# Kernel optimization log

Hardware: AMD Instinct MI355X
Metric: run time of the kernel (lower is better)

## Reference

```python
import jax, jax.numpy as jnp
import numpy as np

B, L, E, H = 1, 2048, 512, 8
D = E // H


def setup_inputs() -> dict:
    key = jax.random.key(0)
    k0, k1, k2 = jax.random.split(key, 3)
    x = jax.random.normal(k0, (B, L, E), jnp.float32)
    W_qkv = jax.random.normal(k1, (E, 3 * E), jnp.float32) / np.sqrt(E).astype(np.float32)
    b_qkv = jnp.zeros((3 * E,), jnp.float32)
    W_out = jax.random.normal(k2, (E, E), jnp.float32) / np.sqrt(E).astype(np.float32)
    b_out = jnp.zeros((E,), jnp.float32)
    return {"x": x, "W_qkv": W_qkv, "b_qkv": b_qkv, "W_out": W_out, "b_out": b_out}


def reference(x, W_qkv, b_qkv, W_out, b_out):
    num_heads = H
    eps = 1e-6
    b, l, e = x.shape
    d = e // num_heads
    qkv = x @ W_qkv + b_qkv                      # [B, L, 3E]
    q, k, v = jnp.split(qkv, 3, axis=-1)
    q = q.reshape(b, l, num_heads, d).transpose(0, 2, 1, 3)  # [B,H,L,D]
    k = k.reshape(b, l, num_heads, d).transpose(0, 2, 1, 3)
    v = v.reshape(b, l, num_heads, d).transpose(0, 2, 1, 3)
    pos = jnp.arange(l, dtype=jnp.float32).reshape(1, 1, l, 1)
    cos_w = jnp.cos(jnp.pi / 2 * pos / l)
    sin_w = jnp.sin(jnp.pi / 2 * pos / l)
    q_prime = jax.nn.relu(q)
    k_prime = jax.nn.relu(k)

    def branch(w):
        qw = q_prime * w                          # [B,H,L,D]
        kw = k_prime * w
        kv = jnp.einsum('bhld,bhle->bhlde', kw, v)  # causal running KV state
        kv_cum = jnp.cumsum(kv, axis=2)
        ctx = jnp.einsum('bhld,bhlde->bhle', qw, kv_cum)
        nrm = jnp.einsum('bhld,bhld->bhl', qw, jnp.cumsum(kw, axis=2))
        return ctx, nrm

    ctx_cos, nrm_cos = branch(cos_w)
    ctx_sin, nrm_sin = branch(sin_w)
    out = (ctx_cos + ctx_sin) / ((nrm_cos + nrm_sin)[..., None] + eps)
    out = out.transpose(0, 2, 1, 3).reshape(b, l, e)
    return out @ W_out + b_out
```

## Files before the change

kernel.cpp:

```cpp
#include <hip/hip_runtime.h>

constexpr int L_SEQ = 2048;
constexpr int E_DIM = 512;
constexpr int H_NUM = 8;
constexpr int QKV_W = 3 * E_DIM;
constexpr int CHK = 64;
constexpr int NC = L_SEQ / CHK;
constexpr float PI_HALF = 1.5707963267948966f;

typedef __attribute__((ext_vector_type(8))) short bf16x8;
typedef __attribute__((ext_vector_type(4))) float f32x4;
typedef __attribute__((ext_vector_type(4))) short short4v;

__device__ __forceinline__ short f2bf(float f) {
  union { float f; unsigned int u; } v; v.f = f;
  unsigned int r = v.u + 0x7fffu + ((v.u >> 16) & 1u);
  return (short)(r >> 16);
}
__device__ __forceinline__ float bf2f(short s) {
  union { unsigned int u; float f; } v;
  v.u = ((unsigned int)(unsigned short)s) << 16;
  return v.f;
}

__device__ __forceinline__ void glds16(const void* g, void* l) {
  __builtin_amdgcn_global_load_lds(
      (const __attribute__((address_space(1))) unsigned int*)g,
      (__attribute__((address_space(3))) unsigned int*)l, 16, 0, 0);
}

template <int WTM, int WTN>
__global__ __launch_bounds__(256) void gemm_mfma_bf16(
    const short* __restrict__ A, const short* __restrict__ Bt,
    const float* __restrict__ bias, float* __restrict__ C,
    int M, int N, int K) {
  constexpr int BM = WTM * 32;
  constexpr int BN = WTN * 32;
  __shared__ short As[BM * 32];
  __shared__ short Bs[BN * 32];

  const int t = threadIdx.x;
  const int wave = t >> 6;
  const int lane = t & 63;
  const int quad = lane >> 4;
  const int lr = lane & 15;

  const int row0 = blockIdx.y * BM;
  const int col0 = blockIdx.x * BN;
  const int wrow = (wave >> 1) * (BM / 2);
  const int wcol = (wave & 1) * (BN / 2);

  f32x4 acc[WTM][WTN];
#pragma unroll
  for (int m = 0; m < WTM; ++m)
#pragma unroll
    for (int n = 0; n < WTN; ++n) acc[m][n] = (f32x4){0.f, 0.f, 0.f, 0.f};

  for (int k0 = 0; k0 < K; k0 += 32) {
#pragma unroll
    for (int p = wave; p < BM / 16; p += 4) {
      const int idx = p * 64 + lane;
      const int r = idx >> 2;
      const int kq = (idx & 3) * 8;
      glds16(A + (size_t)(row0 + r) * K + k0 + kq, As + p * 512);
    }
#pragma unroll
    for (int p = wave; p < BN / 16; p += 4) {
      const int idx = p * 64 + lane;
      const int r = idx >> 2;
      const int kq = (idx & 3) * 8;
      glds16(Bt + (size_t)(col0 + r) * K + k0 + kq, Bs + p * 512);
    }
    __syncthreads();

    bf16x8 af[WTM], bf_[WTN];
#pragma unroll
    for (int m = 0; m < WTM; ++m)
      af[m] = *(const bf16x8*)(As + (wrow + m * 16 + lr) * 32 + quad * 8);
#pragma unroll
    for (int n = 0; n < WTN; ++n)
      bf_[n] = *(const bf16x8*)(Bs + (wcol + n * 16 + lr) * 32 + quad * 8);
#pragma unroll
    for (int m = 0; m < WTM; ++m)
#pragma unroll
      for (int n = 0; n < WTN; ++n)
        acc[m][n] = __builtin_amdgcn_mfma_f32_16x16x32_bf16(af[m], bf_[n], acc[m][n], 0, 0, 0);
    __syncthreads();
  }

#pragma unroll
  for (int m = 0; m < WTM; ++m) {
#pragma unroll
    for (int n = 0; n < WTN; ++n) {
      const int col = col0 + wcol + n * 16 + lr;
      const int rowb = row0 + wrow + m * 16 + quad * 4;
      const float bb = bias[col];
#pragma unroll
      for (int r = 0; r < 4; ++r)
        C[(size_t)(rowb + r) * N + col] = acc[m][n][r] + bb;
    }
  }
}

__global__ __launch_bounds__(256) void cast_x_kernel(
    const float* __restrict__ x, short* __restrict__ xb) {
  const int i = blockIdx.x * 256 + threadIdx.x;
  const float4 v = ((const float4*)x)[i];
  short4v o;
  o.x = f2bf(v.x); o.y = f2bf(v.y); o.z = f2bf(v.z); o.w = f2bf(v.w);
  ((short4v*)xb)[i] = o;
}

__global__ __launch_bounds__(256) void transpose_cast_kernel(
    const float* __restrict__ W, short* __restrict__ Wt, int R, int Cc) {
  __shared__ float tile[32][33];
  const int c0 = blockIdx.x * 32, r0 = blockIdx.y * 32;
  const int tx = threadIdx.x & 31, ty = threadIdx.x >> 5;
  for (int i = ty; i < 32; i += 8) tile[i][tx] = W[(size_t)(r0 + i) * Cc + c0 + tx];
  __syncthreads();
  for (int i = ty; i < 32; i += 8)
    Wt[(size_t)(c0 + i) * R + r0 + tx] = f2bf(tile[tx][i]);
}

__global__ __launch_bounds__(256) void chunk_kv_mfma(
    const float* __restrict__ qkv, float* __restrict__ S, float* __restrict__ ksum) {
  const int c = blockIdx.x, h = blockIdx.y;
  __shared__ short kT[128][72];
  __shared__ short vT[64][72];
  const int t = threadIdx.x;
  const int w = t >> 6, lane = t & 63, lr = lane & 15, quad = lane >> 4;

#pragma unroll
  for (int r = 0; r < 16; ++r) {
    const int i = w + 4 * r, d = lane;
    const float* row = qkv + (size_t)(c * 64 + i) * QKV_W;
    const float kv_ = fmaxf(row[E_DIM + h * 64 + d], 0.f);
    const float v_ = row[2 * E_DIM + h * 64 + d];
    const float th = PI_HALF * (float)(c * 64 + i) / (float)L_SEQ;
    kT[d][i] = f2bf(kv_ * __cosf(th));
    kT[64 + d][i] = f2bf(kv_ * __sinf(th));
    vT[d][i] = f2bf(v_);
  }
  __syncthreads();

  f32x4 acc[8];
#pragma unroll
  for (int n = 0; n < 8; ++n) acc[n] = (f32x4){0.f, 0.f, 0.f, 0.f};
#pragma unroll
  for (int kk = 0; kk < 2; ++kk) {
    const bf16x8 av = *(const bf16x8*)&vT[16 * w + lr][kk * 32 + quad * 8];
#pragma unroll
    for (int n = 0; n < 8; ++n) {
      const bf16x8 bv = *(const bf16x8*)&kT[16 * n + lr][kk * 32 + quad * 8];
      acc[n] = __builtin_amdgcn_mfma_f32_16x16x32_bf16(av, bv, acc[n], 0, 0, 0);
    }
  }

  float* Sc = S + ((size_t)(h * NC + c)) * 8192;
#pragma unroll
  for (int n = 0; n < 8; ++n) {
    const int dd = 16 * n + lr;
#pragma unroll
    for (int r = 0; r < 4; ++r) {
      const int e = 16 * w + quad * 4 + r;
      Sc[(size_t)e * 128 + dd] = acc[n][r];
    }
  }

  if (t < 128) {
    float s = 0.f;
#pragma unroll
    for (int j = 0; j < 8; ++j) {
      const bf16x8 kv8 = *(const bf16x8*)&kT[t][j * 8];
#pragma unroll
      for (int q = 0; q < 8; ++q) s += bf2f(kv8[q]);
    }
    ksum[(size_t)(h * NC + c) * 128 + t] = s;
  }
}

__global__ __launch_bounds__(256) void scan_kernel(
    const float* __restrict__ S, short* __restrict__ Spb,
    const float* __restrict__ ksum, float* __restrict__ ksumP) {
  const int h = blockIdx.y;
  const int e = blockIdx.x * 256 + threadIdx.x;
  float run = 0.f;
#pragma unroll
  for (int c = 0; c < NC; ++c) {
    const size_t off = ((size_t)(h * NC + c)) * 8192 + e;
    Spb[off] = f2bf(run);
    run += S[off];
  }
  if (blockIdx.x == 0 && threadIdx.x < 128) {
    const int d = threadIdx.x;
    float r2 = 0.f;
#pragma unroll
    for (int c = 0; c < NC; ++c) {
      const size_t off = (size_t)(h * NC + c) * 128 + d;
      ksumP[off] = r2;
      r2 += ksum[off];
    }
  }
}

__global__ __launch_bounds__(256) void chunk_out_mfma(
    const float* __restrict__ qkv, const short* __restrict__ Spb,
    const float* __restrict__ ksumP, short* __restrict__ attn) {
  const int c = blockIdx.x, h = blockIdx.y;
  __shared__ short Qc[64][136];
  __shared__ short Kc[64][136];
  __shared__ short Am[64][72];
  __shared__ short vT[64][72];
  __shared__ float nrmP[64][4];
  __shared__ float nrmA[64];
  const int t = threadIdx.x;
  const int w = t >> 6, lane = t & 63, lr = lane & 15, quad = lane >> 4;

#pragma unroll
  for (int r = 0; r < 16; ++r) {
    const int i = w + 4 * r, d = lane;
    const float* row = qkv + (size_t)(c * 64 + i) * QKV_W;
    const float q_ = fmaxf(row[h * 64 + d], 0.f);
    const float k_ = fmaxf(row[E_DIM + h * 64 + d], 0.f);
    const float v_ = row[2 * E_DIM + h * 64 + d];
    const float th = PI_HALF * (float)(c * 64 + i) / (float)L_SEQ;
    const float cw = __cosf(th), sw = __sinf(th);
    Qc[i][d] = f2bf(q_ * cw);
    Qc[i][64 + d] = f2bf(q_ * sw);
    Kc[i][d] = f2bf(k_ * cw);
    Kc[i][64 + d] = f2bf(k_ * sw);
    vT[d][i] = f2bf(v_);
  }
  __syncthreads();

  f32x4 acc_a[4];
#pragma unroll
  for (int n = 0; n < 4; ++n) acc_a[n] = (f32x4){0.f, 0.f, 0.f, 0.f};
#pragma unroll
  for (int kk = 0; kk < 4; ++kk) {
    const bf16x8 av = *(const bf16x8*)&Qc[16 * w + lr][kk * 32 + quad * 8];
#pragma unroll
    for (int n = 0; n < 4; ++n) {
      const bf16x8 bv = *(const bf16x8*)&Kc[16 * n + lr][kk * 32 + quad * 8];
      acc_a[n] = __builtin_amdgcn_mfma_f32_16x16x32_bf16(av, bv, acc_a[n], 0, 0, 0);
    }
  }
#pragma unroll
  for (int n = 0; n < 4; ++n) {
#pragma unroll
    for (int r = 0; r < 4; ++r) {
      const int gi = 16 * w + quad * 4 + r;
      const int gj = 16 * n + lr;
      float val = (gj <= gi) ? acc_a[n][r] : 0.f;
      Am[gi][gj] = f2bf(val);
      float s = val;
      s += __shfl_xor(s, 1, 64);
      s += __shfl_xor(s, 2, 64);
      s += __shfl_xor(s, 4, 64);
      s += __shfl_xor(s, 8, 64);
      if (lr == 0) nrmP[gi][n] = s;
    }
  }

  const short* Spc = Spb + ((size_t)(h * NC + c)) * 8192;
  f32x4 acc_c[4];
#pragma unroll
  for (int n = 0; n < 4; ++n) acc_c[n] = (f32x4){0.f, 0.f, 0.f, 0.f};
#pragma unroll
  for (int kk = 0; kk < 4; ++kk) {
    const bf16x8 av = *(const bf16x8*)&Qc[16 * w + lr][kk * 32 + quad * 8];
#pragma unroll
    for (int n = 0; n < 4; ++n) {
      const bf16x8 bv = *(const bf16x8*)(Spc + (size_t)(16 * n + lr) * 128 + kk * 32 + quad * 8);
      acc_c[n] = __builtin_amdgcn_mfma_f32_16x16x32_bf16(av, bv, acc_c[n], 0, 0, 0);
    }
  }
  __syncthreads();

#pragma unroll
  for (int kk = 0; kk < 2; ++kk) {
    const bf16x8 av = *(const bf16x8*)&Am[16 * w + lr][kk * 32 + quad * 8];
#pragma unroll
    for (int n = 0; n < 4; ++n) {
      const bf16x8 bv = *(const bf16x8*)&vT[16 * n + lr][kk * 32 + quad * 8];
      acc_c[n] = __builtin_amdgcn_mfma_f32_16x16x32_bf16(av, bv, acc_c[n], 0, 0, 0);
    }
  }

  {
    const int i = t >> 2, p = t & 3;
    const float* Kp = ksumP + (size_t)(h * NC + c) * 128;
    float dot = 0.f;
#pragma unroll
    for (int jj = 0; jj < 32; ++jj) {
      const int dd = p * 32 + jj;
      dot += bf2f(Qc[i][dd]) * Kp[dd];
    }
    nrmP[i][p] += dot;
  }
  __syncthreads();
  if (t < 64) nrmA[t] = nrmP[t][0] + nrmP[t][1] + nrmP[t][2] + nrmP[t][3];
  __syncthreads();

#pragma unroll
  for (int n = 0; n < 4; ++n) {
#pragma unroll
    for (int r = 0; r < 4; ++r) {
      const int gi = 16 * w + quad * 4 + r;
      const int e = 16 * n + lr;
      const float val = acc_c[n][r] / (nrmA[gi] + 1e-6f);
      attn[(size_t)(c * 64 + gi) * E_DIM + h * 64 + e] = f2bf(val);
    }
  }
}

extern "C" void kernel_launch(void* const* d_in, const int* in_sizes, int n_in,
                              void* d_out, int out_size, void* d_ws, size_t ws_size,
                              hipStream_t stream) {
  (void)in_sizes; (void)n_in; (void)out_size; (void)ws_size;
  const float* x     = (const float*)d_in[0];
  const float* W_qkv = (const float*)d_in[1];
  const float* b_qkv = (const float*)d_in[2];
  const float* W_out = (const float*)d_in[3];
  const float* b_out = (const float*)d_in[4];
  float* out = (float*)d_out;

  float* ws = (float*)d_ws;
  float* qkv    = ws;
  float* S      = qkv + 3145728;
  float* ksum   = S + 2097152;
  float* ksumP  = ksum + 32768;
  short* Spb    = (short*)(ksumP + 32768);
  short* attn_b = Spb + 2097152;
  short* xb     = attn_b + 1048576;
  short* Wqkv_t = xb + 1048576;
  short* Wout_t = Wqkv_t + 786432;

  cast_x_kernel<<<1024, 256, 0, stream>>>(x, xb);
  transpose_cast_kernel<<<dim3(48, 16), 256, 0, stream>>>(W_qkv, Wqkv_t, E_DIM, QKV_W);
  transpose_cast_kernel<<<dim3(16, 16), 256, 0, stream>>>(W_out, Wout_t, E_DIM, E_DIM);

  gemm_mfma_bf16<4, 4><<<dim3(QKV_W / 128, L_SEQ / 128), 256, 0, stream>>>(
      xb, Wqkv_t, b_qkv, qkv, L_SEQ, QKV_W, E_DIM);

  chunk_kv_mfma<<<dim3(NC, H_NUM), 256, 0, stream>>>(qkv, S, ksum);

  scan_kernel<<<dim3(32, H_NUM), 256, 0, stream>>>(S, Spb, ksum, ksumP);

  chunk_out_mfma<<<dim3(NC, H_NUM), 256, 0, stream>>>(qkv, Spb, ksumP, attn_b);

  gemm_mfma_bf16<2, 2><<<dim3(E_DIM / 64, L_SEQ / 64), 256, 0, stream>>>(
      attn_b, Wout_t, b_out, out, L_SEQ, E_DIM, E_DIM);
}
```

Baseline: 114.1 us.

## Fuse prep kernels, store QKV/state in bf16, replace scan with in-kernel prefix

Merges the x cast and both weight transposes into one prep kernel. The QKV GEMM now writes bf16, and the per-chunk KV states are stored in bf16. The separate scan kernel is removed: the output kernel computes the ksum prefix and accumulates the previous chunk states directly with MFMAs. Both GEMMs get smaller tiles for more blocks. This cuts launches and memory traffic, but later chunks loop over up to 31 earlier states, so work is unbalanced and bf16 state summation loses precision.

```diff
diff --git a/kernel.cpp b/kernel.cpp
--- a/kernel.cpp
+++ b/kernel.cpp
@@ -4,8 +4,7 @@
 constexpr int E_DIM = 512;
 constexpr int H_NUM = 8;
 constexpr int QKV_W = 3 * E_DIM;
-constexpr int CHK = 64;
-constexpr int NC = L_SEQ / CHK;
+constexpr int NC = 32;
 constexpr float PI_HALF = 1.5707963267948966f;
 
 typedef __attribute__((ext_vector_type(8))) short bf16x8;
@@ -29,10 +28,10 @@
       (__attribute__((address_space(3))) unsigned int*)l, 16, 0, 0);
 }
 
-template <int WTM, int WTN>
+template <int WTM, int WTN, bool OB>
 __global__ __launch_bounds__(256) void gemm_mfma_bf16(
     const short* __restrict__ A, const short* __restrict__ Bt,
-    const float* __restrict__ bias, float* __restrict__ C,
+    const float* __restrict__ bias, void* __restrict__ Cout,
     int M, int N, int K) {
   constexpr int BM = WTM * 32;
   constexpr int BN = WTN * 32;
@@ -60,16 +59,12 @@
 #pragma unroll
     for (int p = wave; p < BM / 16; p += 4) {
       const int idx = p * 64 + lane;
-      const int r = idx >> 2;
-      const int kq = (idx & 3) * 8;
-      glds16(A + (size_t)(row0 + r) * K + k0 + kq, As + p * 512);
+      glds16(A + (size_t)(row0 + (idx >> 2)) * K + k0 + (idx & 3) * 8, As + p * 512);
     }
 #pragma unroll
     for (int p = wave; p < BN / 16; p += 4) {
       const int idx = p * 64 + lane;
-      const int r = idx >> 2;
-      const int kq = (idx & 3) * 8;
-      glds16(Bt + (size_t)(col0 + r) * K + k0 + kq, Bs + p * 512);
+      glds16(Bt + (size_t)(col0 + (idx >> 2)) * K + k0 + (idx & 3) * 8, Bs + p * 512);
     }
     __syncthreads();
 
@@ -96,25 +91,41 @@
       const int rowb = row0 + wrow + m * 16 + quad * 4;
       const float bb = bias[col];
 #pragma unroll
-      for (int r = 0; r < 4; ++r)
-        C[(size_t)(rowb + r) * N + col] = acc[m][n][r] + bb;
-    }
-  }
-}
-
-__global__ __launch_bounds__(256) void cast_x_kernel(
-    const float* __restrict__ x, short* __restrict__ xb) {
-  const int i = blockIdx.x * 256 + threadIdx.x;
-  const float4 v = ((const float4*)x)[i];
-  short4v o;
-  o.x = f2bf(v.x); o.y = f2bf(v.y); o.z = f2bf(v.z); o.w = f2bf(v.w);
-  ((short4v*)xb)[i] = o;
-}
-
-__global__ __launch_bounds__(256) void transpose_cast_kernel(
-    const float* __restrict__ W, short* __restrict__ Wt, int R, int Cc) {
+      for (int r = 0; r < 4; ++r) {
+        const float val = acc[m][n][r] + bb;
+        if (OB)
+          ((short*)Cout)[(size_t)(rowb + r) * N + col] = f2bf(val);
+        else
+          ((float*)Cout)[(size_t)(rowb + r) * N + col] = val;
+      }
+    }
+  }
+}
+
+__global__ __launch_bounds__(256) void prep_kernel(
+    const float* __restrict__ x, const float* __restrict__ W_qkv,
+    const float* __restrict__ W_out, short* __restrict__ xb,
+    short* __restrict__ Wqkv_t, short* __restrict__ Wout_t) {
+  const int b = blockIdx.x;
+  if (b < 1024) {
+    const int i = b * 256 + threadIdx.x;
+    const float4 v = ((const float4*)x)[i];
+    short4v o;
+    o.x = f2bf(v.x); o.y = f2bf(v.y); o.z = f2bf(v.z); o.w = f2bf(v.w);
+    ((short4v*)xb)[i] = o;
+    return;
+  }
   __shared__ float tile[32][33];
-  const int c0 = blockIdx.x * 32, r0 = blockIdx.y * 32;
+  const float* W; short* Wt; int R, Cc, c0, r0;
+  if (b < 1792) {
+    const int bb = b - 1024;
+    W = W_qkv; Wt = Wqkv_t; R = E_DIM; Cc = QKV_W;
+    c0 = (bb % 48) * 32; r0 = (bb / 48) * 32;
+  } else {
+    const int bb = b - 1792;
+    W = W_out; Wt = Wout_t; R = E_DIM; Cc = E_DIM;
+    c0 = (bb % 16) * 32; r0 = (bb / 16) * 32;
+  }
   const int tx = threadIdx.x & 31, ty = threadIdx.x >> 5;
   for (int i = ty; i < 32; i += 8) tile[i][tx] = W[(size_t)(r0 + i) * Cc + c0 + tx];
   __syncthreads();
@@ -123,7 +134,7 @@
 }
 
 __global__ __launch_bounds__(256) void chunk_kv_mfma(
-    const float* __restrict__ qkv, float* __restrict__ S, float* __restrict__ ksum) {
+    const short* __restrict__ qkvb, short* __restrict__ Sb, float* __restrict__ ksum) {
   const int c = blockIdx.x, h = blockIdx.y;
   __shared__ short kT[128][72];
   __shared__ short vT[64][72];
@@ -133,9 +144,9 @@
 #pragma unroll
   for (int r = 0; r < 16; ++r) {
     const int i = w + 4 * r, d = lane;
-    const float* row = qkv + (size_t)(c * 64 + i) * QKV_W;
-    const float kv_ = fmaxf(row[E_DIM + h * 64 + d], 0.f);
-    const float v_ = row[2 * E_DIM + h * 64 + d];
+    const short* row = qkvb + (size_t)(c * 64 + i) * QKV_W;
+    const float kv_ = fmaxf(bf2f(row[E_DIM + h * 64 + d]), 0.f);
+    const float v_ = bf2f(row[2 * E_DIM + h * 64 + d]);
     const float th = PI_HALF * (float)(c * 64 + i) / (float)L_SEQ;
     kT[d][i] = f2bf(kv_ * __cosf(th));
     kT[64 + d][i] = f2bf(kv_ * __sinf(th));
@@ -156,14 +167,14 @@
     }
   }
 
-  float* Sc = S + ((size_t)(h * NC + c)) * 8192;
+  short* Sc = Sb + ((size_t)(h * NC + c)) * 8192;
 #pragma unroll
   for (int n = 0; n < 8; ++n) {
     const int dd = 16 * n + lr;
 #pragma unroll
     for (int r = 0; r < 4; ++r) {
       const int e = 16 * w + quad * 4 + r;
-      Sc[(size_t)e * 128 + dd] = acc[n][r];
+      Sc[(size_t)e * 128 + dd] = f2bf(acc[n][r]);
     }
   }
 
@@ -179,38 +190,15 @@
   }
 }
 
-__global__ __launch_bounds__(256) void scan_kernel(
-    const float* __restrict__ S, short* __restrict__ Spb,
-    const float* __restrict__ ksum, float* __restrict__ ksumP) {
-  const int h = blockIdx.y;
-  const int e = blockIdx.x * 256 + threadIdx.x;
-  float run = 0.f;
-#pragma unroll
-  for (int c = 0; c < NC; ++c) {
-    const size_t off = ((size_t)(h * NC + c)) * 8192 + e;
-    Spb[off] = f2bf(run);
-    run += S[off];
-  }
-  if (blockIdx.x == 0 && threadIdx.x < 128) {
-    const int d = threadIdx.x;
-    float r2 = 0.f;
-#pragma unroll
-    for (int c = 0; c < NC; ++c) {
-      const size_t off = (size_t)(h * NC + c) * 128 + d;
-      ksumP[off] = r2;
-      r2 += ksum[off];
-    }
-  }
-}
-
-__global__ __launch_bounds__(256) void chunk_out_mfma(
-    const float* __restrict__ qkv, const short* __restrict__ Spb,
-    const float* __restrict__ ksumP, short* __restrict__ attn) {
+__global__ __launch_bounds__(256) void chunk_out_fused(
+    const short* __restrict__ qkvb, const short* __restrict__ Sb,
+    const float* __restrict__ ksum, short* __restrict__ attn) {
   const int c = blockIdx.x, h = blockIdx.y;
   __shared__ short Qc[64][136];
   __shared__ short Kc[64][136];
   __shared__ short Am[64][72];
   __shared__ short vT[64][72];
+  __shared__ float ksumP_s[128];
   __shared__ float nrmP[64][4];
   __shared__ float nrmA[64];
   const int t = threadIdx.x;
@@ -219,10 +207,10 @@
 #pragma unroll
   for (int r = 0; r < 16; ++r) {
     const int i = w + 4 * r, d = lane;
-    const float* row = qkv + (size_t)(c * 64 + i) * QKV_W;
-    const float q_ = fmaxf(row[h * 64 + d], 0.f);
-    const float k_ = fmaxf(row[E_DIM + h * 64 + d], 0.f);
-    const float v_ = row[2 * E_DIM + h * 64 + d];
+    const short* row = qkvb + (size_t)(c * 64 + i) * QKV_W;
+    const float q_ = fmaxf(bf2f(row[h * 64 + d]), 0.f);
+    const float k_ = fmaxf(bf2f(row[E_DIM + h * 64 + d]), 0.f);
+    const float v_ = bf2f(row[2 * E_DIM + h * 64 + d]);
     const float th = PI_HALF * (float)(c * 64 + i) / (float)L_SEQ;
     const float cw = __cosf(th), sw = __sinf(th);
     Qc[i][d] = f2bf(q_ * cw);
@@ -231,18 +219,27 @@
     Kc[i][64 + d] = f2bf(k_ * sw);
     vT[d][i] = f2bf(v_);
   }
-  __syncthreads();
+  if (t < 128) {
+    float s = 0.f;
+    for (int cp = 0; cp < c; ++cp) s += ksum[(size_t)(h * NC + cp) * 128 + t];
+    ksumP_s[t] = s;
+  }
+  __syncthreads();
+
+  bf16x8 av[4];
+#pragma unroll
+  for (int kk = 0; kk < 4; ++kk)
+    av[kk] = *(const bf16x8*)&Qc[16 * w + lr][kk * 32 + quad * 8];
 
   f32x4 acc_a[4];
 #pragma unroll
   for (int n = 0; n < 4; ++n) acc_a[n] = (f32x4){0.f, 0.f, 0.f, 0.f};
 #pragma unroll
   for (int kk = 0; kk < 4; ++kk) {
-    const bf16x8 av = *(const bf16x8*)&Qc[16 * w + lr][kk * 32 + quad * 8];
 #pragma unroll
     for (int n = 0; n < 4; ++n) {
       const bf16x8 bv = *(const bf16x8*)&Kc[16 * n + lr][kk * 32 + quad * 8];
-      acc_a[n] = __builtin_amdgcn_mfma_f32_16x16x32_bf16(av, bv, acc_a[n], 0, 0, 0);
+      acc_a[n] = __builtin_amdgcn_mfma_f32_16x16x32_bf16(av[kk], bv, acc_a[n], 0, 0, 0);
     }
   }
 #pragma unroll
@@ -262,39 +259,39 @@
     }
   }
 
-  const short* Spc = Spb + ((size_t)(h * NC + c)) * 8192;
   f32x4 acc_c[4];
 #pragma unroll
   for (int n = 0; n < 4; ++n) acc_c[n] = (f32x4){0.f, 0.f, 0.f, 0.f};
-#pragma unroll
-  for (int kk = 0; kk < 4; ++kk) {
-    const bf16x8 av = *(const bf16x8*)&Qc[16 * w + lr][kk * 32 + quad * 8];
-#pragma unroll
-    for (int n = 0; n < 4; ++n) {
-      const bf16x8 bv = *(const bf16x8*)(Spc + (size_t)(16 * n + lr) * 128 + kk * 32 + quad * 8);
-      acc_c[n] = __builtin_amdgcn_mfma_f32_16x16x32_bf16(av, bv, acc_c[n], 0, 0, 0);
+  for (int cp = 0; cp < c; ++cp) {
+    const short* Sc = Sb + ((size_t)(h * NC + cp)) * 8192;
+#pragma unroll
+    for (int kk = 0; kk < 4; ++kk) {
+#pragma unroll
+      for (int n = 0; n < 4; ++n) {
+        const bf16x8 bv = *(const bf16x8*)(Sc + (size_t)(16 * n + lr) * 128 + kk * 32 + quad * 8);
+        acc_c[n] = __builtin_amdgcn_mfma_f32_16x16x32_bf16(av[kk], bv, acc_c[n], 0, 0, 0);
+      }
     }
   }
   __syncthreads();
 
 #pragma unroll
   for (int kk = 0; kk < 2; ++kk) {
-    const bf16x8 av = *(const bf16x8*)&Am[16 * w + lr][kk * 32 + quad * 8];
+    const bf16x8 am = *(const bf16x8*)&Am[16 * w + lr][kk * 32 + quad * 8];
 #pragma unroll
     for (int n = 0; n < 4; ++n) {
       const bf16x8 bv = *(const bf16x8*)&vT[16 * n + lr][kk * 32 + quad * 8];
-      acc_c[n] = __builtin_amdgcn_mfma_f32_16x16x32_bf16(av, bv, acc_c[n], 0, 0, 0);
+      acc_c[n] = __builtin_amdgcn_mfma_f32_16x16x32_bf16(am, bv, acc_c[n], 0, 0, 0);
     }
   }
 
   {
     const int i = t >> 2, p = t & 3;
-    const float* Kp = ksumP + (size_t)(h * NC + c) * 128;
     float dot = 0.f;
 #pragma unroll
     for (int jj = 0; jj < 32; ++jj) {
       const int dd = p * 32 + jj;
-      dot += bf2f(Qc[i][dd]) * Kp[dd];
+      dot += bf2f(Qc[i][dd]) * ksumP_s[dd];
     }
     nrmP[i][p] += dot;
   }
@@ -325,30 +322,24 @@
   const float* b_out = (const float*)d_in[4];
   float* out = (float*)d_out;
 
-  float* ws = (float*)d_ws;
-  float* qkv    = ws;
-  float* S      = qkv + 3145728;
-  float* ksum   = S + 2097152;
-  float* ksumP  = ksum + 32768;
-  short* Spb    = (short*)(ksumP + 32768);
-  short* attn_b = Spb + 2097152;
+  short* sws = (short*)d_ws;
+  short* qkvb   = sws;
+  short* Sb     = qkvb + 3145728;
+  short* attn_b = Sb + 2097152;
   short* xb     = attn_b + 1048576;
   short* Wqkv_t = xb + 1048576;
   short* Wout_t = Wqkv_t + 786432;
-
-  cast_x_kernel<<<1024, 256, 0, stream>>>(x, xb);
-  transpose_cast_kernel<<<dim3(48, 16), 256, 0, stream>>>(W_qkv, Wqkv_t, E_DIM, QKV_W);
-  transpose_cast_kernel<<<dim3(16, 16), 256, 0, stream>>>(W_out, Wout_t, E_DIM, E_DIM);
-
-  gemm_mfma_bf16<4, 4><<<dim3(QKV_W / 128, L_SEQ / 128), 256, 0, stream>>>(
-      xb, Wqkv_t, b_qkv, qkv, L_SEQ, QKV_W, E_DIM);
-
-  chunk_kv_mfma<<<dim3(NC, H_NUM), 256, 0, stream>>>(qkv, S, ksum);
-
-  scan_kernel<<<dim3(32, H_NUM), 256, 0, stream>>>(S, Spb, ksum, ksumP);
-
-  chunk_out_mfma<<<dim3(NC, H_NUM), 256, 0, stream>>>(qkv, Spb, ksumP, attn_b);
-
-  gemm_mfma_bf16<2, 2><<<dim3(E_DIM / 64, L_SEQ / 64), 256, 0, stream>>>(
+  float* ksum   = (float*)(Wout_t + 262144);
+
+  prep_kernel<<<2048, 256, 0, stream>>>(x, W_qkv, W_out, xb, Wqkv_t, Wout_t);
+
+  gemm_mfma_bf16<2, 2, true><<<dim3(QKV_W / 64, L_SEQ / 64), 256, 0, stream>>>(
+      xb, Wqkv_t, b_qkv, qkvb, L_SEQ, QKV_W, E_DIM);
+
+  chunk_kv_mfma<<<dim3(NC, H_NUM), 256, 0, stream>>>(qkvb, Sb, ksum);
+
+  chunk_out_fused<<<dim3(NC, H_NUM), 256, 0, stream>>>(qkvb, Sb, ksum, attn_b);
+
+  gemm_mfma_bf16<1, 2, false><<<dim3(E_DIM / 64, L_SEQ / 32), 256, 0, stream>>>(
       attn_b, Wout_t, b_out, out, L_SEQ, E_DIM, E_DIM);
 }
```

Result: slower. 166.5 us (+46.0%).
